# Kernel optimization log

Measured on AMD Instinct MI355X. Metric: run time of the kernel, lower is better.

Reference implementation:

```python
import jax, jax.numpy as jnp
import numpy as np

B, S, IN, OUT = 4, 2048, 4096, 11008


def setup_inputs() -> dict:
    key = jax.random.key(0)
    k1, k2, k3, k4 = jax.random.split(key, 4)
    x = jax.random.normal(k1, (B, S, IN), dtype=jnp.float32)
    # int8 weight codes (stored as int32 for portability; values in [0,127))
    weight_int8 = jax.random.randint(k2, (OUT, IN), 0, 127, dtype=jnp.int32)
    scale = jax.random.uniform(k3, (OUT,), dtype=jnp.float32) * 0.01 + 1e-4
    bias = jax.random.normal(k4, (OUT,), dtype=jnp.float32)
    return {"x": x, "weight_int8": weight_int8, "scale": scale, "bias": bias}


def reference(x, weight_int8, scale, bias):
    # dequantize: int8 codes -> fp, per-output-row scale (scale.view(-1,1) in torch)
    w = weight_int8.astype(jnp.float32) * scale[:, None]  # [OUT, IN]
    # F.linear(x, w, bias) == x @ w.T + bias
    out = jnp.einsum('bsi,oi->bso', x, w) + bias  # [B, S, OUT]
    return out
```

## Files before the change

kernel.cpp:

```cpp
#include <hip/hip_runtime.h>
#include <hip/hip_bf16.h>
#include <stdint.h>


#define MT 8192
#define KT 4096
#define NT 11008
#define NKT 32
#define MTILES 32
#define NTILES 43
#define CHUNK_BYTES 32768

typedef __attribute__((ext_vector_type(8))) short short8;
typedef __attribute__((ext_vector_type(4))) float f32x4;
typedef __attribute__((ext_vector_type(4))) int i32x4;
typedef __attribute__((ext_vector_type(16))) int i32x16;
typedef __attribute__((ext_vector_type(16))) char char16;

static __device__ __forceinline__ short f2bf(float f) {
  union { float f; unsigned u; } c; c.f = f;
  unsigned u = c.u;
  return (short)((u + 0x7fffu + ((u >> 16) & 1u)) >> 16);
}

__global__ __launch_bounds__(256) void quant_x_kernel(const float* __restrict__ in,
                                                      char* __restrict__ Aws,
                                                      float* __restrict__ sx) {
  const int m = blockIdx.x;
  const int t = threadIdx.x;
  const float* row = in + (size_t)m * KT + t * 16;
  f32x4 v[4];
  float mx = 0.f;
#pragma unroll
  for (int i = 0; i < 4; i++) {
    v[i] = *(const f32x4*)(row + i * 4);
#pragma unroll
    for (int j = 0; j < 4; j++) mx = fmaxf(mx, fabsf(v[i][j]));
  }
#pragma unroll
  for (int off = 32; off; off >>= 1) mx = fmaxf(mx, __shfl_xor(mx, off));
  __shared__ float smx[4];
  if ((t & 63) == 0) smx[t >> 6] = mx;
  __syncthreads();
  mx = fmaxf(fmaxf(smx[0], smx[1]), fmaxf(smx[2], smx[3]));
  const float inv = 127.0f / mx;
  if (t == 0) sx[m] = mx * (1.0f / 127.0f);
  char16 q;
#pragma unroll
  for (int i = 0; i < 4; i++)
#pragma unroll
    for (int j = 0; j < 4; j++) q[i * 4 + j] = (char)(int)rintf(v[i][j] * inv);
  const int mt = m >> 8, r = m & 255, kt = t >> 3, g = t & 7;
  *(char16*)(Aws + ((size_t)mt * NKT + kt) * CHUNK_BYTES + r * 128 +
             ((g * 16) ^ ((r & 7) << 4))) = q;
}

__global__ __launch_bounds__(256) void cvt_w8_kernel(const int* __restrict__ in,
                                                     char* __restrict__ Bws) {
  const int n = blockIdx.x;
  const int t = threadIdx.x;
  const int* s = in + (size_t)n * KT + t * 16;
  char16 q;
#pragma unroll
  for (int i = 0; i < 4; i++) {
    i32x4 a = *(const i32x4*)(s + i * 4);
#pragma unroll
    for (int j = 0; j < 4; j++) q[i * 4 + j] = (char)a[j];
  }
  const int nt = n >> 8, r = n & 255, kt = t >> 3, g = t & 7;
  *(char16*)(Bws + ((size_t)nt * NKT + kt) * CHUNK_BYTES + r * 128 +
             ((g * 16) ^ ((r & 7) << 4))) = q;
}


#define GLD(chunk, j, ldsbase)                                                   \
  __builtin_amdgcn_global_load_lds(                                              \
      (const __attribute__((address_space(1))) void*)((chunk) + (j) * 8192 +     \
                                                      tid * 16),                 \
      (__attribute__((address_space(3))) void*)((ldsbase) + (j) * 8192 +         \
                                                wid * 1024),                     \
      16, 0, 0)

#define BAR asm volatile("s_barrier" ::: "memory")
#define VMC0 asm volatile("s_waitcnt vmcnt(0)" ::: "memory")
#define LGK0 asm volatile("s_waitcnt lgkmcnt(0)" ::: "memory")

#define KOFF(s) ((((s) * 32) + khalf) ^ swz)

#define LDSL(LAp, s, aset, bset)                                \
  do {                                                          \
    const int ko_ = KOFF(s);                                    \
    aset[0] = *(const i32x4*)((LAp) + aoff + ko_);              \
    aset[1] = *(const i32x4*)((LAp) + aoff + 4096 + ko_);       \
    aset[2] = *(const i32x4*)((LAp) + aoff + 8192 + ko_);       \
    aset[3] = *(const i32x4*)((LAp) + aoff + 12288 + ko_);      \
    bset[0] = *(const i32x4*)((LAp) + boff + ko_);              \
    bset[1] = *(const i32x4*)((LAp) + boff + 4096 + ko_);       \
  } while (0)

#define MMS(aset, bset)                                                        \
  do {                                                                         \
    __builtin_amdgcn_s_setprio(1);                                             \
    _Pragma("unroll") for (int mb = 0; mb < 4; mb++)                           \
        _Pragma("unroll") for (int nb = 0; nb < 2; nb++)                       \
            acc[mb][nb] = __builtin_amdgcn_mfma_i32_32x32x32_i8(               \
                aset[mb], bset[nb], acc[mb][nb], 0, 0, 0);                     \
    __builtin_amdgcn_s_setprio(0);                                             \
  } while (0)

__global__ __launch_bounds__(512, 2) void gemm256(
    const char* __restrict__ Aws, const char* __restrict__ Bws,
    const float* __restrict__ sx, const float* __restrict__ scale,
    const float* __restrict__ bias, float* __restrict__ out) {
  extern __shared__ char Lsm[];
  const int tid = threadIdx.x;
  const int lane = tid & 63;
  const int wid = tid >> 6;
  const int wr = wid >> 2;
  const int wc = wid & 3;

  const int bid = blockIdx.x;
  const int lid = (bid & 7) * 172 + (bid >> 3);
  const int g8 = lid / 344;
  const int r8 = lid - g8 * 344;
  const int mt = g8 * 8 + (r8 & 7);
  const int nt = r8 >> 3;

  const char* Ach = Aws + (size_t)mt * NKT * CHUNK_BYTES;
  const char* Bch = Bws + (size_t)nt * NKT * CHUNK_BYTES;

  const int aoff = (wr * 128 + (lane & 31)) * 128;
  const int boff = 32768 + (wc * 64 + (lane & 31)) * 128;
  const int khalf = (lane >> 5) * 16;
  const int swz = (lane & 7) << 4;

  i32x16 acc[4][2] = {};
  i32x4 a0[4], a1[4], b0[2], b1[2];

  {
    char* lA0 = Lsm;
    char* lB0 = Lsm + 32768;
    GLD(Bch, 0, lB0); GLD(Bch, 1, lB0); GLD(Bch, 2, lB0); GLD(Bch, 3, lB0);
    GLD(Ach, 0, lA0); GLD(Ach, 1, lA0); GLD(Ach, 2, lA0); GLD(Ach, 3, lA0);
    VMC0;
    BAR;
    const char* A1 = Ach + CHUNK_BYTES;
    const char* B1 = Bch + CHUNK_BYTES;
    char* lA1 = Lsm + 65536;
    char* lB1 = Lsm + 65536 + 32768;
    GLD(B1, 0, lB1); GLD(B1, 1, lB1); GLD(B1, 2, lB1); GLD(B1, 3, lB1);
    GLD(A1, 0, lA1); GLD(A1, 1, lA1); GLD(A1, 2, lA1); GLD(A1, 3, lA1);
    LDSL(Lsm, 0, a0, b0);
  }

  for (int t = 0; t < NKT; ++t) {
    const char* LA = Lsm + (t & 1) * 65536;

    LDSL(LA, 1, a1, b1);  MMS(a0, b0);
    LDSL(LA, 2, a0, b0);  MMS(a1, b1);
    LDSL(LA, 3, a1, b1);  MMS(a0, b0);
    MMS(a1, b1);

    LGK0;
    VMC0;
    BAR;

    if (t + 1 < NKT) {
      const char* LAn = Lsm + ((t + 1) & 1) * 65536;
      if (t + 2 < NKT) {
        char* dA = Lsm + (t & 1) * 65536;
        char* dB = dA + 32768;
        const char* A2 = Ach + 2 * CHUNK_BYTES;
        const char* B2 = Bch + 2 * CHUNK_BYTES;
        GLD(B2, 0, dB); GLD(B2, 1, dB); GLD(B2, 2, dB); GLD(B2, 3, dB);
        GLD(A2, 0, dA); GLD(A2, 1, dA); GLD(A2, 2, dA); GLD(A2, 3, dA);
      }
      LDSL(LAn, 0, a0, b0);
    }
    Ach += CHUNK_BYTES;
    Bch += CHUNK_BYTES;
  }

  const int col0 = nt * 256 + wc * 64 + (lane & 31);
  const int row0 = mt * 256 + wr * 128 + ((lane >> 5) << 2);
#pragma unroll
  for (int mb = 0; mb < 4; mb++) {
    f32x4 sxq[4];
#pragma unroll
    for (int g = 0; g < 4; g++)
      sxq[g] = *(const f32x4*)(sx + row0 + mb * 32 + g * 8);
#pragma unroll
    for (int nb = 0; nb < 2; nb++) {
      const int n = col0 + nb * 32;
      const float sc = scale[n];
      const float bs = bias[n];
#pragma unroll
      for (int g = 0; g < 4; g++)
#pragma unroll
        for (int j = 0; j < 4; j++) {
          const int row = row0 + mb * 32 + g * 8 + j;
          out[(size_t)row * NT + n] =
              (float)acc[mb][nb][g * 4 + j] * (sxq[g][j] * sc) + bs;
        }
    }
  }
}

__global__ __launch_bounds__(256) void gemm_fallback(
    const float* __restrict__ Ap, const int* __restrict__ Bp,
    const float* __restrict__ scale, const float* __restrict__ bias,
    float* __restrict__ out) {
  __shared__ short ldsA[128 * 64];
  __shared__ short ldsB[128 * 64];
  const int tid = threadIdx.x;
  const int lane = tid & 63;
  const int wid = tid >> 6;
  const int nbn = NT / 128;
  const int cpx = ((MT / 128) * nbn) / 8;
  const int bid = blockIdx.x;
  const int wg = (bid & 7) * cpx + (bid >> 3);
  const int brow = (wg / nbn) * 128;
  const int bcol = (wg % nbn) * 128;
  const int wr = wid >> 1, wc = wid & 1;
  f32x4 acc[4][4] = {{{0.f, 0.f, 0.f, 0.f}}};
  const int srow = tid >> 3;
  const int sk8 = (tid & 7) * 8;
  for (int k0 = 0; k0 < KT; k0 += 64) {
    __syncthreads();
#pragma unroll
    for (int p = 0; p < 4; p++) {
      const int row = p * 32 + srow;
      const float* s = Ap + (size_t)(brow + row) * KT + k0 + sk8;
      f32x4 lo = *(const f32x4*)s;
      f32x4 hi = *(const f32x4*)(s + 4);
      short8 v;
#pragma unroll
      for (int j = 0; j < 4; j++) { v[j] = f2bf(lo[j]); v[4 + j] = f2bf(hi[j]); }
      int bo = (row * 64 + sk8) * 2;
      bo ^= ((row & 7) << 4);
      *(short8*)((char*)ldsA + bo) = v;
    }
#pragma unroll
    for (int p = 0; p < 4; p++) {
      const int row = p * 32 + srow;
      const int* s = Bp + (size_t)(bcol + row) * KT + k0 + sk8;
      i32x4 lo = *(const i32x4*)s;
      i32x4 hi = *(const i32x4*)(s + 4);
      short8 v;
#pragma unroll
      for (int j = 0; j < 4; j++) { v[j] = f2bf((float)lo[j]); v[4 + j] = f2bf((float)hi[j]); }
      int bo = (row * 64 + sk8) * 2;
      bo ^= ((row & 7) << 4);
      *(short8*)((char*)ldsB + bo) = v;
    }
    __syncthreads();
#pragma unroll
    for (int kk = 0; kk < 2; kk++) {
      short8 af[4], bf2[4];
#pragma unroll
      for (int mi = 0; mi < 4; mi++) {
        const int row = wr * 64 + mi * 16 + (lane & 15);
        int bo = (row * 64 + kk * 32 + (lane >> 4) * 8) * 2;
        bo ^= ((row & 7) << 4);
        af[mi] = *(const short8*)((const char*)ldsA + bo);
      }
#pragma unroll
      for (int ni = 0; ni < 4; ni++) {
        const int row = wc * 64 + ni * 16 + (lane & 15);
        int bo = (row * 64 + kk * 32 + (lane >> 4) * 8) * 2;
        bo ^= ((row & 7) << 4);
        bf2[ni] = *(const short8*)((const char*)ldsB + bo);
      }
#pragma unroll
      for (int mi = 0; mi < 4; mi++)
#pragma unroll
        for (int ni = 0; ni < 4; ni++)
          acc[mi][ni] = __builtin_amdgcn_mfma_f32_16x16x32_bf16(af[mi], bf2[ni],
                                                                acc[mi][ni], 0, 0, 0);
    }
  }
#pragma unroll
  for (int ni = 0; ni < 4; ni++) {
    const int n = bcol + wc * 64 + ni * 16 + (lane & 15);
    const float sc = scale[n];
    const float bs = bias[n];
#pragma unroll
    for (int mi = 0; mi < 4; mi++) {
      const int m0 = brow + wr * 64 + mi * 16 + ((lane >> 4) << 2);
#pragma unroll
      for (int j = 0; j < 4; j++)
        out[(size_t)(m0 + j) * NT + n] = acc[mi][ni][j] * sc + bs;
    }
  }
}

extern "C" void kernel_launch(void* const* d_in, const int* in_sizes, int n_in,
                              void* d_out, int out_size, void* d_ws, size_t ws_size,
                              hipStream_t stream) {
  const float* x = (const float*)d_in[0];
  const int* w = (const int*)d_in[1];
  const float* scale = (const float*)d_in[2];
  const float* bias = (const float*)d_in[3];
  float* out = (float*)d_out;

  const size_t a_bytes = (size_t)MTILES * NKT * CHUNK_BYTES;
  const size_t b_bytes = (size_t)NTILES * NKT * CHUNK_BYTES;
  const size_t s_bytes = (size_t)MT * sizeof(float);

  if (ws_size >= a_bytes + b_bytes + s_bytes) {
    char* aw = (char*)d_ws;
    char* bw = aw + a_bytes;
    float* sx = (float*)(bw + b_bytes);
    quant_x_kernel<<<dim3(MT), dim3(256), 0, stream>>>(x, aw, sx);
    cvt_w8_kernel<<<dim3(NT), dim3(256), 0, stream>>>(w, bw);
    hipFuncSetAttribute((const void*)gemm256,
                        hipFuncAttributeMaxDynamicSharedMemorySize, 131072);
    gemm256<<<dim3(MTILES * NTILES), dim3(512), 131072, stream>>>(
        aw, bw, sx, scale, bias, out);
  } else {
    gemm_fallback<<<dim3((MT / 128) * (NT / 128)), dim3(256), 0, stream>>>(
        x, w, scale, bias, out);
  }
}
```

Baseline: 483.0 us.

## Use 4 waves per block with 128x128 per-wave tiles in int8 GEMM

Cuts the GEMM block from 8 waves to 4, so each wave now computes a 128x128 output sub-tile (4x4 MFMA 32x32 accumulators) instead of 128x64. Global-to-LDS loads are split into eight 4KB pieces per operand to cover the same 32KB chunk with fewer threads. The LDS fragment load for the next stage now comes before the prefetch issue, and the explicit lgkmcnt wait is removed. This raises per-wave register reuse and lowers LDS read traffic per MFMA, but doubles accumulator registers and leaves fewer waves to hide latency.

```diff
diff --git a/kernel.cpp b/kernel.cpp
--- a/kernel.cpp
+++ b/kernel.cpp
@@ -75,40 +75,51 @@
 
 #define GLD(chunk, j, ldsbase)                                                   \
   __builtin_amdgcn_global_load_lds(                                              \
-      (const __attribute__((address_space(1))) void*)((chunk) + (j) * 8192 +     \
+      (const __attribute__((address_space(1))) void*)((chunk) + (j) * 4096 +     \
                                                       tid * 16),                 \
-      (__attribute__((address_space(3))) void*)((ldsbase) + (j) * 8192 +         \
+      (__attribute__((address_space(3))) void*)((ldsbase) + (j) * 4096 +         \
                                                 wid * 1024),                     \
       16, 0, 0)
 
+#define GLDALL(Achunk, Bchunk, dA, dB)                                         \
+  do {                                                                         \
+    GLD(Bchunk, 0, dB); GLD(Bchunk, 1, dB); GLD(Bchunk, 2, dB);                \
+    GLD(Bchunk, 3, dB); GLD(Bchunk, 4, dB); GLD(Bchunk, 5, dB);                \
+    GLD(Bchunk, 6, dB); GLD(Bchunk, 7, dB);                                    \
+    GLD(Achunk, 0, dA); GLD(Achunk, 1, dA); GLD(Achunk, 2, dA);                \
+    GLD(Achunk, 3, dA); GLD(Achunk, 4, dA); GLD(Achunk, 5, dA);                \
+    GLD(Achunk, 6, dA); GLD(Achunk, 7, dA);                                    \
+  } while (0)
+
 #define BAR asm volatile("s_barrier" ::: "memory")
 #define VMC0 asm volatile("s_waitcnt vmcnt(0)" ::: "memory")
-#define LGK0 asm volatile("s_waitcnt lgkmcnt(0)" ::: "memory")
 
 #define KOFF(s) ((((s) * 32) + khalf) ^ swz)
 
-#define LDSL(LAp, s, aset, bset)                                \
-  do {                                                          \
-    const int ko_ = KOFF(s);                                    \
-    aset[0] = *(const i32x4*)((LAp) + aoff + ko_);              \
-    aset[1] = *(const i32x4*)((LAp) + aoff + 4096 + ko_);       \
-    aset[2] = *(const i32x4*)((LAp) + aoff + 8192 + ko_);       \
-    aset[3] = *(const i32x4*)((LAp) + aoff + 12288 + ko_);      \
-    bset[0] = *(const i32x4*)((LAp) + boff + ko_);              \
-    bset[1] = *(const i32x4*)((LAp) + boff + 4096 + ko_);       \
+#define LDSL(LAp, s, aset, bset)                             \
+  do {                                                       \
+    const int ko_ = KOFF(s);                                 \
+    aset[0] = *(const i32x4*)((LAp) + aoff + ko_);           \
+    aset[1] = *(const i32x4*)((LAp) + aoff + 4096 + ko_);    \
+    aset[2] = *(const i32x4*)((LAp) + aoff + 8192 + ko_);    \
+    aset[3] = *(const i32x4*)((LAp) + aoff + 12288 + ko_);   \
+    bset[0] = *(const i32x4*)((LAp) + boff + ko_);           \
+    bset[1] = *(const i32x4*)((LAp) + boff + 4096 + ko_);    \
+    bset[2] = *(const i32x4*)((LAp) + boff + 8192 + ko_);    \
+    bset[3] = *(const i32x4*)((LAp) + boff + 12288 + ko_);   \
   } while (0)
 
 #define MMS(aset, bset)                                                        \
   do {                                                                         \
     __builtin_amdgcn_s_setprio(1);                                             \
     _Pragma("unroll") for (int mb = 0; mb < 4; mb++)                           \
-        _Pragma("unroll") for (int nb = 0; nb < 2; nb++)                       \
+        _Pragma("unroll") for (int nb = 0; nb < 4; nb++)                       \
             acc[mb][nb] = __builtin_amdgcn_mfma_i32_32x32x32_i8(               \
                 aset[mb], bset[nb], acc[mb][nb], 0, 0, 0);                     \
     __builtin_amdgcn_s_setprio(0);                                             \
   } while (0)
 
-__global__ __launch_bounds__(512, 2) void gemm256(
+__global__ __launch_bounds__(256, 1) void gemm256(
     const char* __restrict__ Aws, const char* __restrict__ Bws,
     const float* __restrict__ sx, const float* __restrict__ scale,
     const float* __restrict__ bias, float* __restrict__ out) {
@@ -116,8 +127,8 @@
   const int tid = threadIdx.x;
   const int lane = tid & 63;
   const int wid = tid >> 6;
-  const int wr = wid >> 2;
-  const int wc = wid & 3;
+  const int wr = wid >> 1;
+  const int wc = wid & 1;
 
   const int bid = blockIdx.x;
   const int lid = (bid & 7) * 172 + (bid >> 3);
@@ -130,26 +141,20 @@
   const char* Bch = Bws + (size_t)nt * NKT * CHUNK_BYTES;
 
   const int aoff = (wr * 128 + (lane & 31)) * 128;
-  const int boff = 32768 + (wc * 64 + (lane & 31)) * 128;
+  const int boff = 32768 + (wc * 128 + (lane & 31)) * 128;
   const int khalf = (lane >> 5) * 16;
   const int swz = (lane & 7) << 4;
 
-  i32x16 acc[4][2] = {};
-  i32x4 a0[4], a1[4], b0[2], b1[2];
+  i32x16 acc[4][4] = {};
+  i32x4 a0[4], a1[4], b0[4], b1[4];
 
   {
-    char* lA0 = Lsm;
-    char* lB0 = Lsm + 32768;
-    GLD(Bch, 0, lB0); GLD(Bch, 1, lB0); GLD(Bch, 2, lB0); GLD(Bch, 3, lB0);
-    GLD(Ach, 0, lA0); GLD(Ach, 1, lA0); GLD(Ach, 2, lA0); GLD(Ach, 3, lA0);
+    GLDALL(Ach, Bch, Lsm, Lsm + 32768);
     VMC0;
     BAR;
     const char* A1 = Ach + CHUNK_BYTES;
     const char* B1 = Bch + CHUNK_BYTES;
-    char* lA1 = Lsm + 65536;
-    char* lB1 = Lsm + 65536 + 32768;
-    GLD(B1, 0, lB1); GLD(B1, 1, lB1); GLD(B1, 2, lB1); GLD(B1, 3, lB1);
-    GLD(A1, 0, lA1); GLD(A1, 1, lA1); GLD(A1, 2, lA1); GLD(A1, 3, lA1);
+    GLDALL(A1, B1, Lsm + 65536, Lsm + 65536 + 32768);
     LDSL(Lsm, 0, a0, b0);
   }
 
@@ -161,27 +166,22 @@
     LDSL(LA, 3, a1, b1);  MMS(a0, b0);
     MMS(a1, b1);
 
-    LGK0;
     VMC0;
     BAR;
 
     if (t + 1 < NKT) {
       const char* LAn = Lsm + ((t + 1) & 1) * 65536;
+      LDSL(LAn, 0, a0, b0);
       if (t + 2 < NKT) {
         char* dA = Lsm + (t & 1) * 65536;
-        char* dB = dA + 32768;
-        const char* A2 = Ach + 2 * CHUNK_BYTES;
-        const char* B2 = Bch + 2 * CHUNK_BYTES;
-        GLD(B2, 0, dB); GLD(B2, 1, dB); GLD(B2, 2, dB); GLD(B2, 3, dB);
-        GLD(A2, 0, dA); GLD(A2, 1, dA); GLD(A2, 2, dA); GLD(A2, 3, dA);
+        GLDALL(Ach + 2 * CHUNK_BYTES, Bch + 2 * CHUNK_BYTES, dA, dA + 32768);
       }
-      LDSL(LAn, 0, a0, b0);
     }
     Ach += CHUNK_BYTES;
     Bch += CHUNK_BYTES;
   }
 
-  const int col0 = nt * 256 + wc * 64 + (lane & 31);
+  const int col0 = nt * 256 + wc * 128 + (lane & 31);
   const int row0 = mt * 256 + wr * 128 + ((lane >> 5) << 2);
 #pragma unroll
   for (int mb = 0; mb < 4; mb++) {
@@ -190,7 +190,7 @@
     for (int g = 0; g < 4; g++)
       sxq[g] = *(const f32x4*)(sx + row0 + mb * 32 + g * 8);
 #pragma unroll
-    for (int nb = 0; nb < 2; nb++) {
+    for (int nb = 0; nb < 4; nb++) {
       const int n = col0 + nb * 32;
       const float sc = scale[n];
       const float bs = bias[n];
@@ -244,7 +244,7 @@
     for (int p = 0; p < 4; p++) {
       const int row = p * 32 + srow;
       const int* s = Bp + (size_t)(bcol + row) * KT + k0 + sk8;
-      i32x4 lo = *(const i32x4*)s;
+      i32x4 lo = *(const i32x4*)(s);
       i32x4 hi = *(const i32x4*)(s + 4);
       short8 v;
 #pragma unroll
@@ -315,7 +315,7 @@
     cvt_w8_kernel<<<dim3(NT), dim3(256), 0, stream>>>(w, bw);
     hipFuncSetAttribute((const void*)gemm256,
                         hipFuncAttributeMaxDynamicSharedMemorySize, 131072);
-    gemm256<<<dim3(MTILES * NTILES), dim3(512), 131072, stream>>>(
+    gemm256<<<dim3(MTILES * NTILES), dim3(256), 131072, stream>>>(
         aw, bw, sx, scale, bias, out);
   } else {
     gemm_fallback<<<dim3((MT / 128) * (NT / 128)), dim3(256), 0, stream>>>(
```

After: 525.1 us. +8.7%, slower.
